# Kernel optimization log

Hardware: AMD Instinct MI355X
Metric: run time of the kernel (lower is better)

Reference implementation:

```python
import jax, jax.numpy as jnp
import numpy as np

B, N, K = 4, 2048, 32
CIN, COUT, M = 64, 64, 8
HID = 16
EPS = 1e-5


def setup_inputs() -> dict:
    key = jax.random.key(0)
    ks = jax.random.split(key, 12)
    inp = {
        "grouped_xyz": jax.random.normal(ks[0], (B, 3, N, K), jnp.float32),
        "grouped_dist": jax.random.uniform(ks[1], (B, N, K), jnp.float32),
        "grouped_norm": jax.random.normal(ks[2], (B, 3, N, K), jnp.float32),
        "grouped_angle": jax.random.normal(ks[3], (B, 3, N, K), jnp.float32),
        "feature": jax.random.normal(ks[4], (B, CIN, N, K), jnp.float32),
        # scorenet conv1 (14->16, 1x1, no bias) + BN params
        "w1": jax.random.normal(ks[5], (HID, 14), jnp.float32) * (2.0 / 14) ** 0.5,
        "g1": jnp.ones((HID,), jnp.float32),
        "b1": jnp.zeros((HID,), jnp.float32),
        # scorenet conv2 (16->M, 1x1, with bias, no last bn)
        "w2": jax.random.normal(ks[6], (M, HID), jnp.float32) * (2.0 / HID) ** 0.5,
        "bias2": jnp.zeros((M,), jnp.float32),
        # weight bank: kaiming on (M, CIN, COUT) -> permute -> (CIN, M*COUT)
        "weightbank": (jax.random.normal(ks[7], (M, CIN, COUT), jnp.float32)
                       * (2.0 / CIN) ** 0.5).transpose(1, 0, 2).reshape(CIN, M * COUT),
        # output BN params
        "gamma": jnp.ones((COUT,), jnp.float32),
        "beta": jnp.zeros((COUT,), jnp.float32),
    }
    return inp


def _bn_train(x, gamma, beta):
    # BatchNorm2d in training mode: stats over (B, N, K) per channel (axis=1)
    mean = x.mean(axis=(0, 2, 3), keepdims=True)
    var = x.var(axis=(0, 2, 3), keepdims=True)
    xn = (x - mean) * jax.lax.rsqrt(var + EPS)
    return xn * gamma[None, :, None, None] + beta[None, :, None, None]


def _softmax_one(x, axis):
    # exp(x) / (1 + sum exp(x)), numerically stable
    m = jax.lax.stop_gradient(x.max(axis=axis, keepdims=True))
    e = jnp.exp(x - m)
    return e / (e.sum(axis=axis, keepdims=True) + jnp.exp(-m))


def reference(grouped_xyz, grouped_dist, grouped_norm, grouped_angle, feature,
              w1, g1, b1, w2, bias2, weightbank, gamma, beta):
    # geometric feature build -> (B, 14, N, K)
    center_norm = jnp.broadcast_to(grouped_norm[..., :1], grouped_norm.shape)
    norm_diff = grouped_norm - center_norm
    norm_ed = jnp.linalg.norm(norm_diff, axis=1, keepdims=True)   # (B,1,N,K)
    xyz_ed = jnp.linalg.norm(grouped_xyz, axis=1, keepdims=True)  # (B,1,N,K)
    xyz = jnp.concatenate(
        [grouped_xyz, xyz_ed, grouped_norm, norm_diff, norm_ed, grouped_angle],
        axis=1) / (1.0 + grouped_dist[:, None, :, :])

    # scorenet: 1x1 conv + BN + ReLU, then 1x1 conv + bias, softmax_one over channels
    h = jnp.einsum('oc,bcnk->bonk', w1, xyz)
    h = jax.nn.relu(_bn_train(h, g1, b1))
    s = jnp.einsum('oc,bcnk->bonk', w2, h) + bias2[None, :, None, None]
    scores = _softmax_one(s, axis=1)                 # (B, M, N, K)
    scores = scores.transpose(0, 2, 3, 1)            # (B, N, K, M)

    # weight-bank matmul + score-weighted combine
    feat = feature.transpose(0, 2, 3, 1)             # (B, N, K, CIN)
    out = (feat @ weightbank).reshape(B, N, K, M, COUT)
    out = jnp.einsum('bnkm,bnkmo->bnko', scores, out)  # (B, N, K, COUT)
    out = out.transpose(0, 3, 1, 2)                  # (B, COUT, N, K)

    out = _bn_train(out, gamma, beta)
    return jax.nn.relu(out)
```

## Files before the change

kernel.cpp:

```cpp
#include <hip/hip_runtime.h>
#include <hip/hip_bf16.h>
#include <math.h>

namespace {

constexpr int Kn   = 32;
constexpr int CIN  = 64;
constexpr int COUT = 64;
constexpr int Mn   = 8;
constexpr int HIDn = 16;
constexpr int NK   = 65536;
constexpr int PTOT = 262144;
constexpr float EPSf = 1e-5f;

constexpr int NBLK = 256;
constexpr int NTHR = 1024;

constexpr int WS_SUM1 = 0;
constexpr int WS_SQ1  = 16;
constexpr int WS_SUM2 = 64;
constexpr int WS_SQ2  = 128;
constexpr int WS_BAR  = 192;
constexpr int WS_TOT  = 256;

typedef short bf16x8  __attribute__((ext_vector_type(8)));
typedef float f32x4   __attribute__((ext_vector_type(4)));
typedef float f32x16  __attribute__((ext_vector_type(16)));

__device__ __forceinline__ short f2bf(float f) {
  union { __hip_bfloat16 h; unsigned short u; } cv;
  cv.h = __float2bfloat16(f);
  return (short)cv.u;
}

__device__ __forceinline__ float ws_ld(const float* p) {
  return __hip_atomic_load(p, __ATOMIC_RELAXED, __HIP_MEMORY_SCOPE_AGENT);
}

__device__ __forceinline__ void gridbar(int* cnt, int tid, int target) {
  __syncthreads();
  if (tid == 0) {
    __hip_atomic_fetch_add(cnt, 1, __ATOMIC_ACQ_REL, __HIP_MEMORY_SCOPE_AGENT);
    while (__hip_atomic_load(cnt, __ATOMIC_ACQUIRE,
                             __HIP_MEMORY_SCOPE_AGENT) < target) {
      __builtin_amdgcn_s_sleep(8);
    }
  }
  __syncthreads();
}

__device__ __forceinline__ void geom_h(
    const float* __restrict__ xyz, const float* __restrict__ dist,
    const float* __restrict__ nrm, const float* __restrict__ ang,
    const float* __restrict__ w1, int b, int rem, float h[HIDn]) {
  const int cbase = rem & ~(Kn - 1);
  float x[14];
  const float invd = 1.0f / (1.0f + dist[b * NK + rem]);
  float xe = 0.f, ne = 0.f;
#pragma unroll
  for (int d = 0; d < 3; ++d) {
    const int base = (b * 3 + d) * NK;
    const float gx = xyz[base + rem];
    const float gn = nrm[base + rem];
    const float cn = nrm[base + cbase];
    const float ga = ang[base + rem];
    const float nd = gn - cn;
    x[d] = gx; x[4 + d] = gn; x[7 + d] = nd; x[11 + d] = ga;
    xe += gx * gx; ne += nd * nd;
  }
  x[3]  = sqrtf(xe);
  x[10] = sqrtf(ne);
#pragma unroll
  for (int i = 0; i < 14; ++i) x[i] *= invd;
#pragma unroll
  for (int o = 0; o < HIDn; ++o) {
    float s = 0.f;
#pragma unroll
    for (int c = 0; c < 14; ++c) s = fmaf(w1[o * 14 + c], x[c], s);
    h[o] = s;
  }
}

__global__ __launch_bounds__(512) void k0_zero(float* __restrict__ ws) {
  if (threadIdx.x < WS_TOT) ws[threadIdx.x] = 0.f;
}

__global__ __launch_bounds__(NTHR, 1) void kmain(
    const float* __restrict__ xyz, const float* __restrict__ dist,
    const float* __restrict__ nrm, const float* __restrict__ ang,
    const float* __restrict__ feature, const float* __restrict__ w1,
    const float* __restrict__ g1, const float* __restrict__ b1,
    const float* __restrict__ w2, const float* __restrict__ bias2,
    const float* __restrict__ wb, const float* __restrict__ gamma,
    const float* __restrict__ beta, float* __restrict__ ws,
    float* __restrict__ out) {
  __shared__ short lds_b[64 * 64 * 8];
  __shared__ unsigned park[16 * NTHR];
  __shared__ float red[16][128];
  __shared__ float bnp[160];

  int* const bar = (int*)(ws + WS_BAR);

  const int tid = threadIdx.x;
  const int l   = tid & 63;
  const int w   = tid >> 6;
  const int lg  = l >> 5;
  const int col = l & 31;

  const int blk = blockIdx.x;
  const int pos = blk * NTHR + tid;
  const int b   = pos >> 16;
  const int rem = pos & (NK - 1);

#pragma unroll
  for (int ff = 0; ff < 4; ++ff) {
    const int fi = w * 4 + ff;
    const int kk = fi >> 1;
    const int ct = fi & 1;
    const int c  = kk * 2 + lg;
    const int o  = ct * 32 + col;
    bf16x8 frag;
#pragma unroll
    for (int j = 0; j < 8; ++j) frag[j] = f2bf(wb[c * 512 + j * 64 + o]);
    *reinterpret_cast<bf16x8*>(&lds_b[(fi * 64 + l) * 8]) = frag;
  }

  float h[HIDn];
  geom_h(xyz, dist, nrm, ang, w1, b, rem, h);
  {
    float v[32];
#pragma unroll
    for (int i = 0; i < 16; ++i) { v[i] = h[i]; v[16 + i] = h[i] * h[i]; }
#pragma unroll
    for (int off = 32; off >= 1; off >>= 1) {
#pragma unroll
      for (int i = 0; i < 32; ++i) v[i] += __shfl_xor(v[i], off);
    }
    float mv = 0.f;
#pragma unroll
    for (int i = 0; i < 32; ++i) { if (l == i) mv = v[i]; }
    if (l < 32) red[w][l] = mv;
    __syncthreads();
    if (tid < 32) {
      float tot = 0.f;
#pragma unroll
      for (int ww = 0; ww < 16; ++ww) tot += red[ww][tid];
      atomicAdd(&ws[WS_SUM1 + tid], tot);
    }
  }

  gridbar(bar, tid, NBLK);

  if (tid < HIDn) {
    const float inv  = 1.0f / (float)PTOT;
    const float mean = ws_ld(&ws[WS_SUM1 + tid]) * inv;
    const float var  = ws_ld(&ws[WS_SQ1 + tid]) * inv - mean * mean;
    const float s    = g1[tid] * rsqrtf(var + EPSf);
    bnp[tid]      = s;
    bnp[16 + tid] = b1[tid] - mean * s;
  }
  __syncthreads();

  unsigned scp[4];
  {
#pragma unroll
    for (int o = 0; o < HIDn; ++o)
      h[o] = fmaxf(fmaf(h[o], bnp[o], bnp[16 + o]), 0.f);
    float s[Mn];
#pragma unroll
    for (int m = 0; m < Mn; ++m) {
      float a = bias2[m];
#pragma unroll
      for (int j = 0; j < HIDn; ++j) a = fmaf(w2[m * HIDn + j], h[j], a);
      s[m] = a;
    }
    float mx = s[0];
#pragma unroll
    for (int m = 1; m < Mn; ++m) mx = fmaxf(mx, s[m]);
    float sc[Mn];
    float ssum = 0.f;
#pragma unroll
    for (int m = 0; m < Mn; ++m) { sc[m] = expf(s[m] - mx); ssum += sc[m]; }
    const float inv = 1.0f / (ssum + expf(-mx));
#pragma unroll
    for (int m = 0; m < Mn; ++m) sc[m] *= inv;
#pragma unroll
    for (int j = 0; j < 4; ++j) {
      scp[j] = (unsigned)(unsigned short)f2bf(sc[2 * j]) |
               ((unsigned)(unsigned short)f2bf(sc[2 * j + 1]) << 16);
    }
  }

  const int wrem = (blk * NTHR + w * 64) & (NK - 1);
  const float* fbase = feature + (size_t)b * CIN * NK + wrem;
  f32x16 acc0, acc1;

#pragma unroll
  for (int grp = 0; grp < 2; ++grp) {
    unsigned s0p[4];
#pragma unroll
    for (int j = 0; j < 4; ++j) s0p[j] = __shfl(scp[j], grp * 32 + col);
#pragma unroll
    for (int i = 0; i < 16; ++i) { acc0[i] = 0.f; acc1[i] = 0.f; }

    const float* fp = fbase + (size_t)lg * NK + grp * 32 + col;
#pragma unroll 8
    for (int kk = 0; kk < 32; ++kk) {
      const float fA = *fp;
      fp += 2 * NK;
      bf16x8 a;
#pragma unroll
      for (int j = 0; j < 4; ++j) {
        const float slo = __uint_as_float(s0p[j] << 16);
        const float shi = __uint_as_float(s0p[j] & 0xffff0000u);
        a[2 * j]     = f2bf(fA * slo);
        a[2 * j + 1] = f2bf(fA * shi);
      }
      const bf16x8 b0 =
          *reinterpret_cast<const bf16x8*>(&lds_b[((kk * 2 + 0) * 64 + l) * 8]);
      const bf16x8 b1 =
          *reinterpret_cast<const bf16x8*>(&lds_b[((kk * 2 + 1) * 64 + l) * 8]);
      acc0 = __builtin_amdgcn_mfma_f32_32x32x16_bf16(a, b0, acc0, 0, 0, 0);
      acc1 = __builtin_amdgcn_mfma_f32_32x32x16_bf16(a, b1, acc1, 0, 0, 0);
    }

    {
      float s0s = 0.f, q0s = 0.f, s1s = 0.f, q1s = 0.f;
#pragma unroll
      for (int i = 0; i < 16; ++i) {
        s0s += acc0[i]; q0s += acc0[i] * acc0[i];
        s1s += acc1[i]; q1s += acc1[i] * acc1[i];
      }
      s0s += __shfl_xor(s0s, 32); q0s += __shfl_xor(q0s, 32);
      s1s += __shfl_xor(s1s, 32); q1s += __shfl_xor(q1s, 32);
      if (l < 32) {
        if (grp == 0) {
          red[w][col]      = s0s; red[w][32 + col] = s1s;
          red[w][64 + col] = q0s; red[w][96 + col] = q1s;
        } else {
          red[w][col]      += s0s; red[w][32 + col] += s1s;
          red[w][64 + col] += q0s; red[w][96 + col] += q1s;
        }
      }
    }

    if (grp == 0) {
#pragma unroll
      for (int i = 0; i < 8; ++i) {
        const unsigned w0 =
            (unsigned)(unsigned short)f2bf(acc0[2 * i]) |
            ((unsigned)(unsigned short)f2bf(acc0[2 * i + 1]) << 16);
        const unsigned w1 =
            (unsigned)(unsigned short)f2bf(acc1[2 * i]) |
            ((unsigned)(unsigned short)f2bf(acc1[2 * i + 1]) << 16);
        park[i * NTHR + tid]       = w0;
        park[(8 + i) * NTHR + tid] = w1;
      }
    }
  }

  __syncthreads();
  if (tid < 128) {
    float tot = 0.f;
#pragma unroll
    for (int ww = 0; ww < 16; ++ww) tot += red[ww][tid];
    atomicAdd(&ws[WS_SUM2 + tid], tot);
  }

  gridbar(bar, tid, 2 * NBLK);

  if (tid < COUT) {
    const float inv  = 1.0f / (float)PTOT;
    const float mean = ws_ld(&ws[WS_SUM2 + tid]) * inv;
    const float var  = ws_ld(&ws[WS_SQ2 + tid]) * inv - mean * mean;
    const float s    = gamma[tid] * rsqrtf(var + EPSf);
    bnp[32 + tid] = s;
    bnp[96 + tid] = beta[tid] - mean * s;
  }
  __syncthreads();

  float* obase = out + (size_t)b * COUT * NK + wrem;
#pragma unroll
  for (int ct = 0; ct < 2; ++ct) {
    const int o = ct * 32 + col;
    const float scl = bnp[32 + o];
    const float sh  = bnp[96 + o];
    float* orow = obase + (size_t)o * NK;
#pragma unroll
    for (int q = 0; q < 4; ++q) {
      f32x4 v1;
#pragma unroll
      for (int i = 0; i < 4; ++i) {
        const float vv = ct ? acc1[q * 4 + i] : acc0[q * 4 + i];
        v1[i] = fmaxf(fmaf(vv, scl, sh), 0.f);
      }
      *reinterpret_cast<f32x4*>(&orow[32 + q * 8 + 4 * lg]) = v1;
      const unsigned wa = park[(ct * 8 + q * 2 + 0) * NTHR + tid];
      const unsigned wb2 = park[(ct * 8 + q * 2 + 1) * NTHR + tid];
      f32x4 v0;
      v0[0] = __uint_as_float(wa << 16);
      v0[1] = __uint_as_float(wa & 0xffff0000u);
      v0[2] = __uint_as_float(wb2 << 16);
      v0[3] = __uint_as_float(wb2 & 0xffff0000u);
#pragma unroll
      for (int i = 0; i < 4; ++i) v0[i] = fmaxf(fmaf(v0[i], scl, sh), 0.f);
      *reinterpret_cast<f32x4*>(&orow[q * 8 + 4 * lg]) = v0;
    }
  }
}

}

extern "C" void kernel_launch(void* const* d_in, const int* in_sizes, int n_in,
                              void* d_out, int out_size, void* d_ws, size_t ws_size,
                              hipStream_t stream) {
  const float* xyz     = (const float*)d_in[0];
  const float* dist    = (const float*)d_in[1];
  const float* nrm     = (const float*)d_in[2];
  const float* ang     = (const float*)d_in[3];
  const float* feature = (const float*)d_in[4];
  const float* w1      = (const float*)d_in[5];
  const float* g1      = (const float*)d_in[6];
  const float* b1      = (const float*)d_in[7];
  const float* w2      = (const float*)d_in[8];
  const float* bias2   = (const float*)d_in[9];
  const float* wb      = (const float*)d_in[10];
  const float* gamma   = (const float*)d_in[11];
  const float* beta    = (const float*)d_in[12];
  float* out = (float*)d_out;
  float* ws  = (float*)d_ws;

  hipLaunchKernelGGL(k0_zero, dim3(1), dim3(512), 0, stream, ws);
  hipLaunchKernelGGL(kmain, dim3(NBLK), dim3(NTHR), 0, stream,
                     xyz, dist, nrm, ang, feature, w1, g1, b1,
                     w2, bias2, wb, gamma, beta, ws, out);
}
```

Measured before the change: 82.49 us.

## Process 32 positions per wave and double grid size, dropping LDS park buffer

Each wave now handles 32 positions instead of 64, and the grid doubles to 512 blocks. This removes the second MFMA group and the bf16 park buffer in LDS that held the first group's results across the grid barrier. Without the 64KB park array, more blocks can be co-resident, and the first-group outputs no longer pass through bf16, which improves accuracy. The cost is that half the lanes sit idle during the geometry/scorenet stage, and twice as many blocks take part in the grid barrier and the atomics.

Result: slower. 202.4 us (+145.4%).

```diff
diff --git a/kernel.cpp b/kernel.cpp
--- a/kernel.cpp
+++ b/kernel.cpp
@@ -13,8 +13,9 @@
 constexpr int PTOT = 262144;
 constexpr float EPSf = 1e-5f;
 
-constexpr int NBLK = 256;
+constexpr int NBLK = 512;
 constexpr int NTHR = 1024;
+constexpr int POSB = 512;
 
 constexpr int WS_SUM1 = 0;
 constexpr int WS_SQ1  = 16;
@@ -85,7 +86,7 @@
   if (threadIdx.x < WS_TOT) ws[threadIdx.x] = 0.f;
 }
 
-__global__ __launch_bounds__(NTHR, 1) void kmain(
+__global__ __launch_bounds__(NTHR, 8) void kmain(
     const float* __restrict__ xyz, const float* __restrict__ dist,
     const float* __restrict__ nrm, const float* __restrict__ ang,
     const float* __restrict__ feature, const float* __restrict__ w1,
@@ -95,7 +96,6 @@
     const float* __restrict__ beta, float* __restrict__ ws,
     float* __restrict__ out) {
   __shared__ short lds_b[64 * 64 * 8];
-  __shared__ unsigned park[16 * NTHR];
   __shared__ float red[16][128];
   __shared__ float bnp[160];
 
@@ -107,10 +107,10 @@
   const int lg  = l >> 5;
   const int col = l & 31;
 
-  const int blk = blockIdx.x;
-  const int pos = blk * NTHR + tid;
-  const int b   = pos >> 16;
-  const int rem = pos & (NK - 1);
+  const int blk  = blockIdx.x;
+  const int pbase = blk * POSB + w * 32;
+  const int b    = pbase >> 16;
+  const int wrem = pbase & (NK - 1);
 
 #pragma unroll
   for (int ff = 0; ff < 4; ++ff) {
@@ -126,7 +126,11 @@
   }
 
   float h[HIDn];
-  geom_h(xyz, dist, nrm, ang, w1, b, rem, h);
+#pragma unroll
+  for (int i = 0; i < HIDn; ++i) h[i] = 0.f;
+  if (l < 32) {
+    geom_h(xyz, dist, nrm, ang, w1, b, (wrem + col) & (NK - 1), h);
+  }
   {
     float v[32];
 #pragma unroll
@@ -191,19 +195,16 @@
     }
   }
 
-  const int wrem = (blk * NTHR + w * 64) & (NK - 1);
-  const float* fbase = feature + (size_t)b * CIN * NK + wrem;
   f32x16 acc0, acc1;
-
-#pragma unroll
-  for (int grp = 0; grp < 2; ++grp) {
+  {
     unsigned s0p[4];
 #pragma unroll
-    for (int j = 0; j < 4; ++j) s0p[j] = __shfl(scp[j], grp * 32 + col);
+    for (int j = 0; j < 4; ++j) s0p[j] = __shfl(scp[j], col);
 #pragma unroll
     for (int i = 0; i < 16; ++i) { acc0[i] = 0.f; acc1[i] = 0.f; }
 
-    const float* fp = fbase + (size_t)lg * NK + grp * 32 + col;
+    const float* fp = feature + (size_t)b * CIN * NK + wrem +
+                      (size_t)lg * NK + col;
 #pragma unroll 8
     for (int kk = 0; kk < 32; ++kk) {
       const float fA = *fp;
@@ -223,48 +224,28 @@
       acc0 = __builtin_amdgcn_mfma_f32_32x32x16_bf16(a, b0, acc0, 0, 0, 0);
       acc1 = __builtin_amdgcn_mfma_f32_32x32x16_bf16(a, b1, acc1, 0, 0, 0);
     }
-
-    {
-      float s0s = 0.f, q0s = 0.f, s1s = 0.f, q1s = 0.f;
-#pragma unroll
-      for (int i = 0; i < 16; ++i) {
-        s0s += acc0[i]; q0s += acc0[i] * acc0[i];
-        s1s += acc1[i]; q1s += acc1[i] * acc1[i];
-      }
-      s0s += __shfl_xor(s0s, 32); q0s += __shfl_xor(q0s, 32);
-      s1s += __shfl_xor(s1s, 32); q1s += __shfl_xor(q1s, 32);
-      if (l < 32) {
-        if (grp == 0) {
-          red[w][col]      = s0s; red[w][32 + col] = s1s;
-          red[w][64 + col] = q0s; red[w][96 + col] = q1s;
-        } else {
-          red[w][col]      += s0s; red[w][32 + col] += s1s;
-          red[w][64 + col] += q0s; red[w][96 + col] += q1s;
-        }
-      }
-    }
-
-    if (grp == 0) {
-#pragma unroll
-      for (int i = 0; i < 8; ++i) {
-        const unsigned w0 =
-            (unsigned)(unsigned short)f2bf(acc0[2 * i]) |
-            ((unsigned)(unsigned short)f2bf(acc0[2 * i + 1]) << 16);
-        const unsigned w1 =
-            (unsigned)(unsigned short)f2bf(acc1[2 * i]) |
-            ((unsigned)(unsigned short)f2bf(acc1[2 * i + 1]) << 16);
-        park[i * NTHR + tid]       = w0;
-        park[(8 + i) * NTHR + tid] = w1;
-      }
-    }
-  }
-
-  __syncthreads();
-  if (tid < 128) {
-    float tot = 0.f;
-#pragma unroll
-    for (int ww = 0; ww < 16; ++ww) tot += red[ww][tid];
-    atomicAdd(&ws[WS_SUM2 + tid], tot);
+  }
+
+  {
+    float s0s = 0.f, q0s = 0.f, s1s = 0.f, q1s = 0.f;
+#pragma unroll
+    for (int i = 0; i < 16; ++i) {
+      s0s += acc0[i]; q0s += acc0[i] * acc0[i];
+      s1s += acc1[i]; q1s += acc1[i] * acc1[i];
+    }
+    s0s += __shfl_xor(s0s, 32); q0s += __shfl_xor(q0s, 32);
+    s1s += __shfl_xor(s1s, 32); q1s += __shfl_xor(q1s, 32);
+    if (l < 32) {
+      red[w][col]      = s0s; red[w][32 + col] = s1s;
+      red[w][64 + col] = q0s; red[w][96 + col] = q1s;
+    }
+    __syncthreads();
+    if (tid < 128) {
+      float tot = 0.f;
+#pragma unroll
+      for (int ww = 0; ww < 16; ++ww) tot += red[ww][tid];
+      atomicAdd(&ws[WS_SUM2 + tid], tot);
+    }
   }
 
   gridbar(bar, tid, 2 * NBLK);
@@ -288,23 +269,13 @@
     float* orow = obase + (size_t)o * NK;
 #pragma unroll
     for (int q = 0; q < 4; ++q) {
-      f32x4 v1;
+      f32x4 v;
 #pragma unroll
       for (int i = 0; i < 4; ++i) {
         const float vv = ct ? acc1[q * 4 + i] : acc0[q * 4 + i];
-        v1[i] = fmaxf(fmaf(vv, scl, sh), 0.f);
+        v[i] = fmaxf(fmaf(vv, scl, sh), 0.f);
       }
-      *reinterpret_cast<f32x4*>(&orow[32 + q * 8 + 4 * lg]) = v1;
-      const unsigned wa = park[(ct * 8 + q * 2 + 0) * NTHR + tid];
-      const unsigned wb2 = park[(ct * 8 + q * 2 + 1) * NTHR + tid];
-      f32x4 v0;
-      v0[0] = __uint_as_float(wa << 16);
-      v0[1] = __uint_as_float(wa & 0xffff0000u);
-      v0[2] = __uint_as_float(wb2 << 16);
-      v0[3] = __uint_as_float(wb2 & 0xffff0000u);
-#pragma unroll
-      for (int i = 0; i < 4; ++i) v0[i] = fmaxf(fmaf(v0[i], scl, sh), 0.f);
-      *reinterpret_cast<f32x4*>(&orow[q * 8 + 4 * lg]) = v0;
+      *reinterpret_cast<f32x4*>(&orow[q * 8 + 4 * lg]) = v;
     }
   }
 }
```
